# Optimization experiments

Measured on AMD Instinct MI355X. Metric: run time of the kernel, lower is better.

The kernel has to match this reference:

```python
import jax, jax.numpy as jnp
import numpy as np

DIM = 2048
N_HEADS = 32
N_KV_HEADS = 8
HEAD_DIM = 64
BATCH = 2
SEQ = 2048
N_REP = N_HEADS // N_KV_HEADS
SCALE = HEAD_DIM ** -0.5
ROPE_BASE = 10000.0


def setup_inputs() -> dict:
    key = jax.random.key(0)
    ks = jax.random.split(key, 5)
    x = jax.random.normal(ks[0], (BATCH, SEQ, DIM), dtype=jnp.float32)
    # weights stored as (in, out) so projection is x @ W
    Wq = jax.random.normal(ks[1], (DIM, N_HEADS * HEAD_DIM), dtype=jnp.float32) * (DIM ** -0.5)
    Wk = jax.random.normal(ks[2], (DIM, N_KV_HEADS * HEAD_DIM), dtype=jnp.float32) * (DIM ** -0.5)
    Wv = jax.random.normal(ks[3], (DIM, N_KV_HEADS * HEAD_DIM), dtype=jnp.float32) * (DIM ** -0.5)
    Wo = jax.random.normal(ks[4], (N_HEADS * HEAD_DIM, DIM), dtype=jnp.float32) * ((N_HEADS * HEAD_DIM) ** -0.5)
    # RoPE tables (seq, head_dim)
    inv_freq = 1.0 / (ROPE_BASE ** (jnp.arange(0, HEAD_DIM, 2, dtype=jnp.float32) / HEAD_DIM))
    t = jnp.arange(SEQ, dtype=jnp.float32)
    freqs = jnp.outer(t, inv_freq)                      # (S, D/2)
    emb = jnp.concatenate([freqs, freqs], axis=-1)      # (S, D)
    cos = jnp.cos(emb)
    sin = jnp.sin(emb)
    # additive causal mask (1,1,S,S)
    neg = jnp.finfo(jnp.float32).min
    causal = jnp.tril(jnp.ones((SEQ, SEQ), dtype=bool))
    attention_mask = jnp.where(causal, 0.0, neg)[None, None, :, :].astype(jnp.float32)
    return {"x": x, "Wq": Wq, "Wk": Wk, "Wv": Wv, "Wo": Wo,
            "cos": cos, "sin": sin, "attention_mask": attention_mask}


def _rotate_half(u):
    h = u.shape[-1] // 2
    return jnp.concatenate([-u[..., h:], u[..., :h]], axis=-1)


def reference(x, Wq, Wk, Wv, Wo, cos, sin, attention_mask):
    b, s, _ = x.shape
    q = (x @ Wq).reshape(b, s, N_HEADS, HEAD_DIM)
    k = (x @ Wk).reshape(b, s, N_KV_HEADS, HEAD_DIM)
    v = (x @ Wv).reshape(b, s, N_KV_HEADS, HEAD_DIM)
    # RoPE, broadcast over head dim (unsqueeze_dim=2)
    c = cos[None, :, None, :]
    sn = sin[None, :, None, :]
    q = q * c + _rotate_half(q) * sn
    k = k * c + _rotate_half(k) * sn
    # repeat KV heads for GQA: (b,s,kvh,d) -> (b,s,h,d)
    k = jnp.repeat(k, N_REP, axis=2)
    v = jnp.repeat(v, N_REP, axis=2)
    # (b,h,s,d)
    q = q.transpose(0, 2, 1, 3)
    k = k.transpose(0, 2, 1, 3)
    v = v.transpose(0, 2, 1, 3)
    scores = jnp.einsum("bhqd,bhkd->bhqk", q, k) * SCALE + attention_mask
    attn = jax.nn.softmax(scores.astype(jnp.float32), axis=-1).astype(q.dtype)
    out = jnp.einsum("bhqk,bhkd->bhqd", attn, v)
    out = out.transpose(0, 2, 1, 3).reshape(b, s, N_HEADS * HEAD_DIM)
    return out @ Wo
```

## Files before the change

### kernel.cpp

```cpp
#include <hip/hip_runtime.h>
#include <hip/hip_bf16.h>

typedef unsigned short u16;
typedef unsigned int   u32;
typedef __bf16 bf16_t;
typedef bf16_t bf16x8 __attribute__((ext_vector_type(8)));
typedef u16    u16x8  __attribute__((ext_vector_type(8)));
typedef float  f32x4  __attribute__((ext_vector_type(4)));

#define DIM  2048
#define SEQ  2048
#define BATCH 2
#define NH   32
#define NKVH 8
#define HD   64
#define KVDIM (NKVH*HD)
#define NQKV (DIM + 2*KVDIM)
#define SCALE 0.125f

__device__ __forceinline__ float b2f(u16 u) {
  union { u32 i; float f; } v; v.i = ((u32)u) << 16; return v.f;
}
__device__ __forceinline__ u16 f2b(float f) {
  union { float f; u32 i; } v; v.f = f;
  u32 x = v.i;
  return (u16)((x + 0x7fffu + ((x >> 16) & 1u)) >> 16);
}
__device__ __forceinline__ u32 pkbf2(float a, float b) {
  __hip_bfloat162 h = __float22bfloat162_rn(float2{a, b});
  union { __hip_bfloat162 h; u32 u; } v; v.h = h; return v.u;
}
__device__ __forceinline__ int probe_bf16(const u32* probe) { return probe[0] != 0u; }
__device__ __forceinline__ float ext_ld(const void* p, long idx, int mode_bf16) {
  return mode_bf16 ? b2f(((const u16*)p)[idx]) : ((const float*)p)[idx];
}
__device__ __forceinline__ void gload_lds16(const u16* g, u16* l) {
  __builtin_amdgcn_global_load_lds((const __attribute__((address_space(1))) void*)g,
                                   (__attribute__((address_space(3))) void*)l, 16, 0, 0);
}

__global__ void cast_x(const void* __restrict__ in, u16* __restrict__ out,
                       const u32* __restrict__ probe) {
  int mode = probe_bf16(probe);
  long base = ((long)blockIdx.x * 256 + threadIdx.x) * 8;
  if (mode) {
    *(uint4*)&out[base] = *(const uint4*)((const u16*)in + base);
  } else {
    float4 f0 = *(const float4*)((const float*)in + base);
    float4 f1 = *(const float4*)((const float*)in + base + 4);
    u16x8 t;
    t[0] = f2b(f0.x); t[1] = f2b(f0.y); t[2] = f2b(f0.z); t[3] = f2b(f0.w);
    t[4] = f2b(f1.x); t[5] = f2b(f1.y); t[6] = f2b(f1.z); t[7] = f2b(f1.w);
    *(u16x8*)&out[base] = t;
  }
}

__global__ void transpose_qkv(const void* __restrict__ Wq, const void* __restrict__ Wk,
                              const void* __restrict__ Wv, u16* __restrict__ out,
                              const u32* __restrict__ probe) {
  int mode = probe_bf16(probe);
  __shared__ u16 t[32][33];
  int xt = blockIdx.x;
  const void* in; int C, c0, obase;
  if (xt < 64)      { in = Wq; C = DIM;   c0 = xt * 32;        obase = 0; }
  else if (xt < 80) { in = Wk; C = KVDIM; c0 = (xt - 64) * 32; obase = DIM; }
  else              { in = Wv; C = KVDIM; c0 = (xt - 80) * 32; obase = DIM + KVDIM; }
  int r0 = blockIdx.y * 32;
  int tx = threadIdx.x, ty = threadIdx.y;
#pragma unroll
  for (int i = 0; i < 32; i += 8)
    t[ty + i][tx] = mode ? ((const u16*)in)[(long)(r0 + ty + i) * C + c0 + tx]
                         : f2b(((const float*)in)[(long)(r0 + ty + i) * C + c0 + tx]);
  __syncthreads();
#pragma unroll
  for (int i = 0; i < 32; i += 8)
    out[(long)(obase + c0 + ty + i) * DIM + r0 + tx] = t[tx][ty + i];
}

__global__ void transpose_w(const void* __restrict__ in, u16* __restrict__ out,
                            int R, int C, const u32* __restrict__ probe) {
  int mode = probe_bf16(probe);
  __shared__ u16 t[32][33];
  int c0 = blockIdx.x * 32, r0 = blockIdx.y * 32;
  int tx = threadIdx.x, ty = threadIdx.y;
#pragma unroll
  for (int i = 0; i < 32; i += 8)
    t[ty + i][tx] = mode ? ((const u16*)in)[(long)(r0 + ty + i) * C + c0 + tx]
                         : f2b(((const float*)in)[(long)(r0 + ty + i) * C + c0 + tx]);
  __syncthreads();
#pragma unroll
  for (int i = 0; i < 32; i += 8)
    out[(long)(c0 + ty + i) * R + r0 + tx] = t[tx][ty + i];
}

__global__ void rope_both(u16* __restrict__ Qb, u16* __restrict__ Kb,
                          const void* __restrict__ cosb, const void* __restrict__ sinb,
                          const u32* __restrict__ probe) {
  int mode = probe_bf16(probe);
  long gid = (long)blockIdx.x * 256 + threadIdx.x;
  const long NQp = (long)BATCH * SEQ * NH * 32;
  u16* base_p; int n_heads; long t; float osc;
  if (gid < NQp) { base_p = Qb; n_heads = NH; t = gid; osc = SCALE; }
  else           { base_p = Kb; n_heads = NKVH; t = gid - NQp; osc = 1.0f; }
  int pair = t & 31;
  long t2 = t >> 5;
  int h = (int)(t2 % n_heads);
  long row = t2 / n_heads;
  int s = (int)(row & (SEQ - 1));
  long base = row * (n_heads * HD) + h * HD + pair;
  float q0 = b2f(base_p[base]), q1 = b2f(base_p[base + 32]);
  float c0 = ext_ld(cosb, (long)s * HD + pair, mode);
  float c1 = ext_ld(cosb, (long)s * HD + pair + 32, mode);
  float s0 = ext_ld(sinb, (long)s * HD + pair, mode);
  float s1 = ext_ld(sinb, (long)s * HD + pair + 32, mode);
  base_p[base]      = f2b((q0 * c0 - q1 * s0) * osc);
  base_p[base + 32] = f2b((q1 * c1 + q0 * s1) * osc);
}


__launch_bounds__(256)
__global__ void gemm_qkv(const void* __restrict__ A, const u16* __restrict__ Bt,
                         u16* __restrict__ Qb, u16* __restrict__ Kb, u16* __restrict__ Vt,
                         int a_half, const u32* __restrict__ probe) {
  int mode = a_half || probe_bf16(probe);
  __shared__ __align__(16) u16 As[128 * 32];
  __shared__ __align__(16) u16 Bs[128 * 32];
  int tid = threadIdx.x, lane = tid & 63, wv = tid >> 6;
  int l16 = lane & 15, q = lane >> 4;
  int bm0 = blockIdx.y * 128, bn0 = blockIdx.x * 128;
  int mbase = (wv & 1) * 64, nbase = (wv >> 1) * 64;
  int c0 = tid, c1 = tid + 256;
  int r0 = c0 >> 2, s0 = (c0 & 3) ^ ((r0 >> 1) & 3);
  int r1 = c1 >> 2, s1 = (c1 & 3) ^ ((r1 >> 1) & 3);
  const int K = DIM;
  long aoff0 = (long)(bm0 + r0) * K + s0 * 8;
  long aoff1 = (long)(bm0 + r1) * K + s1 * 8;
  long boff0 = (long)(bn0 + r0) * K + s0 * 8;
  long boff1 = (long)(bn0 + r1) * K + s1 * 8;
  int rsw = (q ^ ((l16 >> 1) & 3)) * 8;
  f32x4 acc[4][4] = {};
  for (int k0 = 0; k0 < K; k0 += 32) {
    __syncthreads();
    if (mode) {
      gload_lds16((const u16*)A + aoff0 + k0, &As[wv * 512]);
      gload_lds16((const u16*)A + aoff1 + k0, &As[2048 + wv * 512]);
    } else {
      const float* Af = (const float*)A;
      float4 f0 = *(const float4*)(Af + aoff0 + k0);
      float4 f1 = *(const float4*)(Af + aoff0 + k0 + 4);
      u16x8 t;
      t[0] = f2b(f0.x); t[1] = f2b(f0.y); t[2] = f2b(f0.z); t[3] = f2b(f0.w);
      t[4] = f2b(f1.x); t[5] = f2b(f1.y); t[6] = f2b(f1.z); t[7] = f2b(f1.w);
      *(u16x8*)&As[c0 * 8] = t;
      float4 g0 = *(const float4*)(Af + aoff1 + k0);
      float4 g1 = *(const float4*)(Af + aoff1 + k0 + 4);
      u16x8 u;
      u[0] = f2b(g0.x); u[1] = f2b(g0.y); u[2] = f2b(g0.z); u[3] = f2b(g0.w);
      u[4] = f2b(g1.x); u[5] = f2b(g1.y); u[6] = f2b(g1.z); u[7] = f2b(g1.w);
      *(u16x8*)&As[c1 * 8] = u;
    }
    gload_lds16(Bt + boff0 + k0, &Bs[wv * 512]);
    gload_lds16(Bt + boff1 + k0, &Bs[2048 + wv * 512]);
    __syncthreads();
    bf16x8 af[4], bfr[4];
#pragma unroll
    for (int mi = 0; mi < 4; mi++)
      af[mi] = *(const bf16x8*)&As[(mbase + mi * 16 + l16) * 32 + rsw];
#pragma unroll
    for (int ni = 0; ni < 4; ni++)
      bfr[ni] = *(const bf16x8*)&Bs[(nbase + ni * 16 + l16) * 32 + rsw];
#pragma unroll
    for (int mi = 0; mi < 4; mi++)
#pragma unroll
      for (int ni = 0; ni < 4; ni++)
        acc[mi][ni] = __builtin_amdgcn_mfma_f32_16x16x32_bf16(
            af[mi], bfr[ni], acc[mi][ni], 0, 0, 0);
  }
  if (bn0 < DIM + KVDIM) {
    u16* Cb; int ldc, ncol0;
    if (bn0 < DIM) { Cb = Qb; ldc = DIM; ncol0 = bn0; }
    else           { Cb = Kb; ldc = KVDIM; ncol0 = bn0 - DIM; }
#pragma unroll
    for (int mi = 0; mi < 4; mi++)
#pragma unroll
      for (int ni = 0; ni < 4; ni++)
#pragma unroll
        for (int r = 0; r < 4; r++) {
          int m = bm0 + mbase + mi * 16 + q * 4 + r;
          int n = ncol0 + nbase + ni * 16 + l16;
          Cb[(long)m * ldc + n] = f2b(acc[mi][ni][r]);
        }
  } else {
    int vcol0 = bn0 - DIM - KVDIM;
#pragma unroll
    for (int mi = 0; mi < 4; mi++)
#pragma unroll
      for (int ni = 0; ni < 4; ni++) {
        int vcol = vcol0 + nbase + ni * 16 + l16;
        int kvh2 = vcol >> 6, d = vcol & 63;
        int m = bm0 + mbase + mi * 16 + q * 4;
        int bb = m >> 11, s = m & (SEQ - 1);
        uint2 w;
        w.x = pkbf2(acc[mi][ni][0], acc[mi][ni][1]);
        w.y = pkbf2(acc[mi][ni][2], acc[mi][ni][3]);
        *(uint2*)&Vt[((long)(bb * NKVH + kvh2) * HD + d) * SEQ + s] = w;
      }
  }
}

__launch_bounds__(256)
__global__ void gemm_ao(const u16* __restrict__ A, const u16* __restrict__ Bt,
                        void* __restrict__ C, const u32* __restrict__ probe) {
  int mode = probe_bf16(probe);
  __shared__ __align__(16) u16 As[128 * 32];
  __shared__ __align__(16) u16 Bs[128 * 32];
  int tid = threadIdx.x, lane = tid & 63, wv = tid >> 6;
  int l16 = lane & 15, q = lane >> 4;
  int bm0 = blockIdx.y * 128, bn0 = blockIdx.x * 128;
  int mbase = (wv & 1) * 64, nbase = (wv >> 1) * 64;
  int c0 = tid, c1 = tid + 256;
  int r0 = c0 >> 2, s0 = (c0 & 3) ^ ((r0 >> 1) & 3);
  int r1 = c1 >> 2, s1 = (c1 & 3) ^ ((r1 >> 1) & 3);
  const int K = DIM;
  long aoff0 = (long)(bm0 + r0) * K + s0 * 8;
  long aoff1 = (long)(bm0 + r1) * K + s1 * 8;
  long boff0 = (long)(bn0 + r0) * K + s0 * 8;
  long boff1 = (long)(bn0 + r1) * K + s1 * 8;
  int rsw = (q ^ ((l16 >> 1) & 3)) * 8;
  f32x4 acc[4][4] = {};
  for (int k0 = 0; k0 < K; k0 += 32) {
    __syncthreads();
    gload_lds16(A + aoff0 + k0, &As[wv * 512]);
    gload_lds16(A + aoff1 + k0, &As[2048 + wv * 512]);
    gload_lds16(Bt + boff0 + k0, &Bs[wv * 512]);
    gload_lds16(Bt + boff1 + k0, &Bs[2048 + wv * 512]);
    __syncthreads();
    bf16x8 af[4], bfr[4];
#pragma unroll
    for (int mi = 0; mi < 4; mi++)
      af[mi] = *(const bf16x8*)&As[(mbase + mi * 16 + l16) * 32 + rsw];
#pragma unroll
    for (int ni = 0; ni < 4; ni++)
      bfr[ni] = *(const bf16x8*)&Bs[(nbase + ni * 16 + l16) * 32 + rsw];
#pragma unroll
    for (int mi = 0; mi < 4; mi++)
#pragma unroll
      for (int ni = 0; ni < 4; ni++)
        acc[mi][ni] = __builtin_amdgcn_mfma_f32_16x16x32_bf16(
            af[mi], bfr[ni], acc[mi][ni], 0, 0, 0);
  }
#pragma unroll
  for (int mi = 0; mi < 4; mi++)
#pragma unroll
    for (int ni = 0; ni < 4; ni++)
#pragma unroll
      for (int r = 0; r < 4; r++) {
        int m = bm0 + mbase + mi * 16 + q * 4 + r;
        int n = bn0 + nbase + ni * 16 + l16;
        if (mode) ((u16*)C)[(long)m * DIM + n] = f2b(acc[mi][ni][r]);
        else      ((float*)C)[(long)m * DIM + n] = acc[mi][ni][r];
      }
}

__launch_bounds__(256, 4)
__global__ void attn_kernel(const u16* __restrict__ Q, const u16* __restrict__ K,
                            const u16* __restrict__ Vt, u16* __restrict__ AO) {
  __shared__ __align__(16) u16 Ks[64 * 64];
  __shared__ __align__(16) u16 Vs[64 * 64];
  __shared__ __align__(16) u16 Ps[4][16 * 64];
  int tid = threadIdx.x, lane = tid & 63, wv = tid >> 6;
  int l16 = lane & 15, q = lane >> 4;
  int i = blockIdx.x;
  int bh = blockIdx.y;
  int b = bh >> 5, h = bh & 31, kvh = h >> 2;
  const u16* Kp = K + (long)b * SEQ * KVDIM + kvh * HD;
  const u16* Vp = Vt + (long)(b * NKVH + kvh) * HD * SEQ;

  int cA = tid, cB = tid + 256;
  int rA = cA >> 3, bA = (cA & 7) ^ (rA & 7);
  int rB = cB >> 3, bB = (cB & 7) ^ (rB & 7);
  const u16* kSrcA = Kp + (long)rA * KVDIM + bA * 8;
  const u16* kSrcB = Kp + (long)rB * KVDIM + bB * 8;
  const u16* vSrcA = Vp + (long)rA * SEQ + bA * 8;
  const u16* vSrcB = Vp + (long)rB * SEQ + bB * 8;
  u16* kDstA = &Ks[(wv * 64 + lane) * 8];
  u16* kDstB = &Ks[(256 + wv * 64 + lane) * 8];
  u16* vDstA = &Vs[(wv * 64 + lane) * 8];
  u16* vDstB = &Vs[(256 + wv * 64 + lane) * 8];

  int e = l16 & 7;
  int off0 = (q ^ e) * 8;
  int off1 = ((4 + q) ^ e) * 8;

  bf16x8 ones;
#pragma unroll
  for (int j = 0; j < 8; j++) ones[j] = (bf16_t)1.0f;

#pragma unroll
  for (int ph = 0; ph < 2; ph++) {
    int t = ph ? (31 - i) : i;
    int qbase = t * 64 + wv * 16;
    const u16* Qp = Q + (long)(b * SEQ + qbase) * DIM + h * HD;
    bf16x8 aq0 = *(const bf16x8*)&Qp[l16 * DIM + q * 8];
    bf16x8 aq1 = *(const bf16x8*)&Qp[l16 * DIM + 32 + q * 8];
    f32x4 o_acc[4] = {};
    f32x4 l_acc = {};
    int qrow = qbase + l16;

    for (int kt = 0; kt <= t; kt++) {
      long kk = (long)kt * 64;
      __syncthreads();
      gload_lds16(kSrcA + kk * KVDIM, kDstA);
      gload_lds16(kSrcB + kk * KVDIM, kDstB);
      gload_lds16(vSrcA + kk, vDstA);
      gload_lds16(vSrcB + kk, vDstB);
      __syncthreads();

      f32x4 sc[4];
#pragma unroll
      for (int ni = 0; ni < 4; ni++) {
        bf16x8 bk0 = *(const bf16x8*)&Ks[(ni * 16 + l16) * 64 + off0];
        bf16x8 bk1 = *(const bf16x8*)&Ks[(ni * 16 + l16) * 64 + off1];
        f32x4 z = {};
        z = __builtin_amdgcn_mfma_f32_16x16x32_bf16(bk0, aq0, z, 0, 0, 0);
        z = __builtin_amdgcn_mfma_f32_16x16x32_bf16(bk1, aq1, z, 0, 0, 0);
        sc[ni] = z;
      }
      if (kt == t) {
#pragma unroll
        for (int ni = 0; ni < 4; ni++)
#pragma unroll
          for (int r = 0; r < 4; r++) {
            int kv = (int)kk + ni * 16 + q * 4 + r;
            float p = __expf(sc[ni][r]);
            sc[ni][r] = (kv <= qrow) ? p : 0.f;
          }
      } else {
#pragma unroll
        for (int ni = 0; ni < 4; ni++)
#pragma unroll
          for (int r = 0; r < 4; r++) sc[ni][r] = __expf(sc[ni][r]);
      }
#pragma unroll
      for (int ni = 0; ni < 4; ni++) {
        uint2 w;
        w.x = pkbf2(sc[ni][0], sc[ni][1]);
        w.y = pkbf2(sc[ni][2], sc[ni][3]);
        int pblk = (2 * ni + (q >> 1)) ^ e;
        *(uint2*)&Ps[wv][l16 * 64 + pblk * 8 + (q & 1) * 4] = w;
      }
      bf16x8 ap0 = *(const bf16x8*)&Ps[wv][l16 * 64 + off0];
      bf16x8 ap1 = *(const bf16x8*)&Ps[wv][l16 * 64 + off1];
      l_acc = __builtin_amdgcn_mfma_f32_16x16x32_bf16(ap0, ones, l_acc, 0, 0, 0);
      l_acc = __builtin_amdgcn_mfma_f32_16x16x32_bf16(ap1, ones, l_acc, 0, 0, 0);
#pragma unroll
      for (int di = 0; di < 4; di++) {
        bf16x8 bv0 = *(const bf16x8*)&Vs[(di * 16 + l16) * 64 + off0];
        bf16x8 bv1 = *(const bf16x8*)&Vs[(di * 16 + l16) * 64 + off1];
        o_acc[di] = __builtin_amdgcn_mfma_f32_16x16x32_bf16(ap0, bv0, o_acc[di], 0, 0, 0);
        o_acc[di] = __builtin_amdgcn_mfma_f32_16x16x32_bf16(ap1, bv1, o_acc[di], 0, 0, 0);
      }
    }
    long obase = (long)(b * SEQ + qbase + q * 4) * DIM + h * HD;
#pragma unroll
    for (int r = 0; r < 4; r++) {
      float inv = 1.0f / l_acc[r];
#pragma unroll
      for (int di = 0; di < 4; di++)
        AO[obase + (long)r * DIM + di * 16 + l16] = f2b(o_acc[di][r] * inv);
    }
  }
}

extern "C" void kernel_launch(void* const* d_in, const int* in_sizes, int n_in,
                              void* d_out, int out_size, void* d_ws, size_t ws_size,
                              hipStream_t stream) {
  const void* x    = d_in[0];
  const void* Wq   = d_in[1];
  const void* Wk   = d_in[2];
  const void* Wv   = d_in[3];
  const void* Wo   = d_in[4];
  const void* cosb = d_in[5];
  const void* sinb = d_in[6];
  const u32*  probe = (const u32*)d_in[7];

  u16* WqkvT = (u16*)d_ws;
  u16* WoT = WqkvT + (size_t)NQKV * DIM;
  u16* Qb  = WoT + (size_t)DIM * DIM;
  u16* Kb  = Qb  + (size_t)BATCH * SEQ * DIM;
  u16* Vt  = Kb  + (size_t)BATCH * SEQ * KVDIM;
  u16* xb  = Vt  + (size_t)BATCH * NKVH * HD * SEQ;
  u16* AO  = Qb;

  size_t need_xb = ((size_t)(xb - WqkvT) + (size_t)BATCH * SEQ * DIM) * sizeof(u16);
  int use_xb = ws_size >= need_xb;

  dim3 blk32(32, 8);
  transpose_qkv<<<dim3(96, 64), blk32, 0, stream>>>(Wq, Wk, Wv, WqkvT, probe);
  transpose_w<<<dim3(DIM / 32, DIM / 32), blk32, 0, stream>>>(Wo, WoT, DIM, DIM, probe);

  int M = BATCH * SEQ;
  if (use_xb) {
    cast_x<<<(M * DIM) / (256 * 8), 256, 0, stream>>>(x, xb, probe);
    gemm_qkv<<<dim3(NQKV / 128, M / 128), 256, 0, stream>>>(xb, WqkvT, Qb, Kb, Vt, 1, probe);
  } else {
    gemm_qkv<<<dim3(NQKV / 128, M / 128), 256, 0, stream>>>(x, WqkvT, Qb, Kb, Vt, 0, probe);
  }

  long rope_slots = (long)M * NH * 32 + (long)M * NKVH * 32;
  rope_both<<<(int)(rope_slots / 256), 256, 0, stream>>>(Qb, Kb, cosb, sinb, probe);

  attn_kernel<<<dim3(16, BATCH * NH), 256, 0, stream>>>(Qb, Kb, Vt, AO);

  gemm_ao<<<dim3(DIM / 128, M / 128), 256, 0, stream>>>(AO, WoT, d_out, probe);
}
```

Measured before the change: 327.2 us.

## Replace QKV and output GEMMs with 8-wave double-buffered pipelined GEMM core

Adds a templated 512-thread GEMM core with 256-wide N tiles, BK=64, LDS double buffering, interleaved async global-to-LDS stages, explicit vmcnt waits, sched barriers and setprio around MFMA quads. The QKV projection and the output projection both use it, replacing the simple single-buffered 128x128 kernels that synchronised twice per 32-wide K step. cast_x now skips work when inputs are already bf16, and the QKV GEMM reads x directly in that case. The change aims to hide load latency and raise MFMA utilisation, at the cost of more LDS per block and tighter hand-tuned wait counts that must match the issue order.

New measurement: 343.8 us. 1.05x slower.

```diff
diff --git a/kernel.cpp b/kernel.cpp
--- a/kernel.cpp
+++ b/kernel.cpp
@@ -42,17 +42,14 @@
 __global__ void cast_x(const void* __restrict__ in, u16* __restrict__ out,
                        const u32* __restrict__ probe) {
   int mode = probe_bf16(probe);
+  if (mode) return;
   long base = ((long)blockIdx.x * 256 + threadIdx.x) * 8;
-  if (mode) {
-    *(uint4*)&out[base] = *(const uint4*)((const u16*)in + base);
-  } else {
-    float4 f0 = *(const float4*)((const float*)in + base);
-    float4 f1 = *(const float4*)((const float*)in + base + 4);
-    u16x8 t;
-    t[0] = f2b(f0.x); t[1] = f2b(f0.y); t[2] = f2b(f0.z); t[3] = f2b(f0.w);
-    t[4] = f2b(f1.x); t[5] = f2b(f1.y); t[6] = f2b(f1.z); t[7] = f2b(f1.w);
-    *(u16x8*)&out[base] = t;
-  }
+  float4 f0 = *(const float4*)((const float*)in + base);
+  float4 f1 = *(const float4*)((const float*)in + base + 4);
+  u16x8 t;
+  t[0] = f2b(f0.x); t[1] = f2b(f0.y); t[2] = f2b(f0.z); t[3] = f2b(f0.w);
+  t[4] = f2b(f1.x); t[5] = f2b(f1.y); t[6] = f2b(f1.z); t[7] = f2b(f1.w);
+  *(u16x8*)&out[base] = t;
 }
 
 __global__ void transpose_qkv(const void* __restrict__ Wq, const void* __restrict__ Wk,
@@ -117,6 +114,221 @@
   base_p[base + 32] = f2b((q1 * c1 + q0 * s1) * osc);
 }
 
+
+#define WAITV(N) asm volatile("s_waitcnt vmcnt(%0)" :: "n"(N) : "memory")
+#define WAITL()  asm volatile("s_waitcnt lgkmcnt(0)" ::: "memory")
+#define BARR()   __builtin_amdgcn_s_barrier()
+#define SCHEDB() __builtin_amdgcn_sched_barrier(0)
+#define PRIO1()  __builtin_amdgcn_s_setprio(1)
+#define PRIO0()  __builtin_amdgcn_s_setprio(0)
+
+#define STAGE_A(h, bufi, kt) do { _Pragma("unroll") \
+  for (int _j = 0; _j < AL; ++_j) \
+    gload_lds16(Ax + aSrcOff[h][_j] + (kt) * 64, (u16*)&As[(bufi) * (BM * 64) + aDst[h][_j]]); } while (0)
+
+#define STAGE_B(h, bufi, kt) do { _Pragma("unroll") \
+  for (int _j = 0; _j < 2; ++_j) \
+    gload_lds16(Bt + bSrcOff[h][_j] + (kt) * 64, (u16*)&Bs[(bufi) * (256 * 64) + bDst[h][_j]]); } while (0)
+
+#define LDA_HALF(Lp, mh) do { _Pragma("unroll") \
+  for (int _m = 0; _m < MH2; ++_m) { \
+    const u16* _r = (Lp) + (wm * WM + (mh) * (WM / 2) + _m * 16 + l16) * 64; \
+    af[_m][0] = *(const bf16x8*)&_r[sw0]; \
+    af[_m][1] = *(const bf16x8*)&_r[sw1]; } } while (0)
+
+#define LDB_HALF(Lp, nh) do { _Pragma("unroll") \
+  for (int _n = 0; _n < 2; ++_n) { \
+    const u16* _r = (Lp) + (wn * 64 + (nh) * 32 + _n * 16 + l16) * 64; \
+    bfr[nh][_n][0] = *(const bf16x8*)&_r[sw0]; \
+    bfr[nh][_n][1] = *(const bf16x8*)&_r[sw1]; } } while (0)
+
+#define MFMA_Q(mh, nh) do { _Pragma("unroll") \
+  for (int _m = 0; _m < MH2; ++_m) \
+    _Pragma("unroll") \
+    for (int _n = 0; _n < 2; ++_n) { \
+      f32x4 _z = acc[(mh) * MH2 + _m][(nh) * 2 + _n]; \
+      _z = __builtin_amdgcn_mfma_f32_16x16x32_bf16(af[_m][0], bfr[nh][_n][0], _z, 0, 0, 0); \
+      _z = __builtin_amdgcn_mfma_f32_16x16x32_bf16(af[_m][1], bfr[nh][_n][1], _z, 0, 0, 0); \
+      acc[(mh) * MH2 + _m][(nh) * 2 + _n] = _z; } } while (0)
+
+template<int BM, int EPI>
+__device__ __forceinline__ void gemm8_core(const u16* __restrict__ Ax, const u16* __restrict__ Bt,
+                                           u16* __restrict__ Qb, u16* __restrict__ Kb,
+                                           u16* __restrict__ Vt, void* __restrict__ Cout,
+                                           const u32* __restrict__ probe) {
+  constexpr int WM  = BM / 2;
+  constexpr int MI  = WM / 16;
+  constexpr int MH2 = MI / 2;
+  constexpr int AL  = BM / 128;
+  constexpr int VM_A = 6 + 3 * AL;
+  constexpr int VM_B = 4 + 4 * AL;
+  constexpr int K = DIM;
+  __shared__ __align__(16) u16 As[2 * BM * 64];
+  __shared__ __align__(16) u16 Bs[2 * 256 * 64];
+
+  int tid = threadIdx.x, lane = tid & 63, wv = tid >> 6;
+  int l16 = lane & 15, q = lane >> 4;
+  int wm = wv >> 2, wn = wv & 3;
+  int bm0 = blockIdx.y * BM, bn0 = blockIdx.x * 256;
+
+  int srow = lane >> 3;
+  int scolb = ((lane & 7) ^ srow) * 8;
+  int e7 = l16 & 7;
+  int sw0 = (q ^ e7) * 8, sw1 = ((4 + q) ^ e7) * 8;
+
+  int aSrcOff[2][AL], aDst[2][AL];
+#pragma unroll
+  for (int h = 0; h < 2; ++h)
+#pragma unroll
+    for (int j = 0; j < AL; ++j) {
+      int g = wv * AL + j;
+      int rb = (BM == 256) ? ((g >> 3) * 128 + h * 64 + (g & 7) * 8)
+                           : ((g >> 2) * 64 + h * 32 + (g & 3) * 8);
+      aSrcOff[h][j] = (bm0 + rb + srow) * K + scolb;
+      aDst[h][j] = rb * 64 + lane * 8;
+    }
+  int bSrcOff[2][2], bDst[2][2];
+#pragma unroll
+  for (int h = 0; h < 2; ++h)
+#pragma unroll
+    for (int j = 0; j < 2; ++j) {
+      int g = wv * 2 + j;
+      int rb = (g >> 2) * 64 + h * 32 + (g & 3) * 8;
+      bSrcOff[h][j] = (bn0 + rb + srow) * K + scolb;
+      bDst[h][j] = rb * 64 + lane * 8;
+    }
+
+  const u16* As0 = As;  const u16* As1 = As + BM * 64;
+  const u16* Bs0 = Bs;  const u16* Bs1 = Bs + 256 * 64;
+
+  f32x4 acc[MI][4] = {};
+  bf16x8 af[MH2][2];
+  bf16x8 bfr[2][2][2];
+
+  STAGE_A(0, 0, 0);
+  STAGE_B(0, 0, 0);
+  STAGE_B(1, 0, 0);
+  STAGE_A(1, 0, 0);
+  STAGE_A(0, 1, 1);
+  STAGE_B(0, 1, 1);
+  STAGE_B(1, 1, 1);
+
+#pragma unroll 1
+  for (int i = 0; i < 16; ++i) {
+    int te = 2 * i + 2; if (te > 31) te = 31;
+    int to = 2 * i + 3; if (to > 31) to = 31;
+    SCHEDB();
+    STAGE_A(1, 1, 2 * i + 1);
+    WAITV(VM_A); BARR(); SCHEDB();
+    LDA_HALF(As0, 0); LDB_HALF(Bs0, 0);
+    WAITL(); BARR();
+    PRIO1(); MFMA_Q(0, 0); PRIO0();
+    SCHEDB();
+    STAGE_A(0, 0, te);
+    WAITV(VM_B); BARR(); SCHEDB();
+    LDB_HALF(Bs0, 1);
+    WAITL(); BARR();
+    PRIO1(); MFMA_Q(0, 1); PRIO0();
+    SCHEDB();
+    STAGE_B(0, 0, te);
+    WAITV(VM_A); BARR(); SCHEDB();
+    LDA_HALF(As0, 1);
+    WAITL(); BARR();
+    PRIO1(); MFMA_Q(1, 0); PRIO0();
+    SCHEDB();
+    STAGE_B(1, 0, te);
+    PRIO1(); MFMA_Q(1, 1); PRIO0();
+    SCHEDB();
+    STAGE_A(1, 0, te);
+    WAITV(VM_A); BARR(); SCHEDB();
+    LDA_HALF(As1, 0); LDB_HALF(Bs1, 0);
+    WAITL(); BARR();
+    PRIO1(); MFMA_Q(0, 0); PRIO0();
+    SCHEDB();
+    STAGE_A(0, 1, to);
+    WAITV(VM_B); BARR(); SCHEDB();
+    LDB_HALF(Bs1, 1);
+    WAITL(); BARR();
+    PRIO1(); MFMA_Q(0, 1); PRIO0();
+    SCHEDB();
+    STAGE_B(0, 1, to);
+    WAITV(VM_A); BARR(); SCHEDB();
+    LDA_HALF(As1, 1);
+    WAITL(); BARR();
+    PRIO1(); MFMA_Q(1, 0); PRIO0();
+    SCHEDB();
+    STAGE_B(1, 1, to);
+    PRIO1(); MFMA_Q(1, 1); PRIO0();
+  }
+
+  if constexpr (EPI == 0) {
+    if (bn0 < DIM) {
+#pragma unroll
+      for (int mi = 0; mi < MI; ++mi)
+#pragma unroll
+        for (int ni = 0; ni < 4; ++ni)
+#pragma unroll
+          for (int r = 0; r < 4; ++r) {
+            int m = bm0 + wm * WM + mi * 16 + q * 4 + r;
+            int n = bn0 + wn * 64 + ni * 16 + l16;
+            Qb[(long)m * DIM + n] = f2b(acc[mi][ni][r]);
+          }
+    } else if (bn0 < DIM + KVDIM) {
+#pragma unroll
+      for (int mi = 0; mi < MI; ++mi)
+#pragma unroll
+        for (int ni = 0; ni < 4; ++ni)
+#pragma unroll
+          for (int r = 0; r < 4; ++r) {
+            int m = bm0 + wm * WM + mi * 16 + q * 4 + r;
+            int n = bn0 - DIM + wn * 64 + ni * 16 + l16;
+            Kb[(long)m * KVDIM + n] = f2b(acc[mi][ni][r]);
+          }
+    } else {
+#pragma unroll
+      for (int mi = 0; mi < MI; ++mi)
+#pragma unroll
+        for (int ni = 0; ni < 4; ++ni) {
+          int vcol = bn0 - (DIM + KVDIM) + wn * 64 + ni * 16 + l16;
+          int kvh2 = vcol >> 6, d = vcol & 63;
+          int m0 = bm0 + wm * WM + mi * 16 + q * 4;
+          int bb = m0 >> 11, s = m0 & (SEQ - 1);
+          uint2 w;
+          w.x = pkbf2(acc[mi][ni][0], acc[mi][ni][1]);
+          w.y = pkbf2(acc[mi][ni][2], acc[mi][ni][3]);
+          *(uint2*)&Vt[((long)(bb * NKVH + kvh2) * HD + d) * SEQ + s] = w;
+        }
+    }
+  } else {
+    int mode = probe_bf16(probe);
+#pragma unroll
+    for (int mi = 0; mi < MI; ++mi)
+#pragma unroll
+      for (int ni = 0; ni < 4; ++ni)
+#pragma unroll
+        for (int r = 0; r < 4; ++r) {
+          int m = bm0 + wm * WM + mi * 16 + q * 4 + r;
+          int n = bn0 + wn * 64 + ni * 16 + l16;
+          long idx = (long)m * DIM + n;
+          if (mode) ((u16*)Cout)[idx] = f2b(acc[mi][ni][r]);
+          else      ((float*)Cout)[idx] = acc[mi][ni][r];
+        }
+  }
+}
+
+__global__ __launch_bounds__(512, 2)
+void gemm_qkv8(const void* __restrict__ x, const u16* __restrict__ xb,
+               const u16* __restrict__ Bt, u16* __restrict__ Qb, u16* __restrict__ Kb,
+               u16* __restrict__ Vt, const u32* __restrict__ probe) {
+  const u16* Ax = probe_bf16(probe) ? (const u16*)x : xb;
+  gemm8_core<256, 0>(Ax, Bt, Qb, Kb, Vt, nullptr, probe);
+}
+
+__global__ __launch_bounds__(512, 2)
+void gemm_ao8(const u16* __restrict__ A, const u16* __restrict__ Bt,
+              void* __restrict__ C, const u32* __restrict__ probe) {
+  gemm8_core<128, 1>(A, Bt, nullptr, nullptr, nullptr, C, probe);
+}
 
 __launch_bounds__(256)
 __global__ void gemm_qkv(const void* __restrict__ A, const u16* __restrict__ Bt,
@@ -208,60 +420,6 @@
   }
 }
 
-__launch_bounds__(256)
-__global__ void gemm_ao(const u16* __restrict__ A, const u16* __restrict__ Bt,
-                        void* __restrict__ C, const u32* __restrict__ probe) {
-  int mode = probe_bf16(probe);
-  __shared__ __align__(16) u16 As[128 * 32];
-  __shared__ __align__(16) u16 Bs[128 * 32];
-  int tid = threadIdx.x, lane = tid & 63, wv = tid >> 6;
-  int l16 = lane & 15, q = lane >> 4;
-  int bm0 = blockIdx.y * 128, bn0 = blockIdx.x * 128;
-  int mbase = (wv & 1) * 64, nbase = (wv >> 1) * 64;
-  int c0 = tid, c1 = tid + 256;
-  int r0 = c0 >> 2, s0 = (c0 & 3) ^ ((r0 >> 1) & 3);
-  int r1 = c1 >> 2, s1 = (c1 & 3) ^ ((r1 >> 1) & 3);
-  const int K = DIM;
-  long aoff0 = (long)(bm0 + r0) * K + s0 * 8;
-  long aoff1 = (long)(bm0 + r1) * K + s1 * 8;
-  long boff0 = (long)(bn0 + r0) * K + s0 * 8;
-  long boff1 = (long)(bn0 + r1) * K + s1 * 8;
-  int rsw = (q ^ ((l16 >> 1) & 3)) * 8;
-  f32x4 acc[4][4] = {};
-  for (int k0 = 0; k0 < K; k0 += 32) {
-    __syncthreads();
-    gload_lds16(A + aoff0 + k0, &As[wv * 512]);
-    gload_lds16(A + aoff1 + k0, &As[2048 + wv * 512]);
-    gload_lds16(Bt + boff0 + k0, &Bs[wv * 512]);
-    gload_lds16(Bt + boff1 + k0, &Bs[2048 + wv * 512]);
-    __syncthreads();
-    bf16x8 af[4], bfr[4];
-#pragma unroll
-    for (int mi = 0; mi < 4; mi++)
-      af[mi] = *(const bf16x8*)&As[(mbase + mi * 16 + l16) * 32 + rsw];
-#pragma unroll
-    for (int ni = 0; ni < 4; ni++)
-      bfr[ni] = *(const bf16x8*)&Bs[(nbase + ni * 16 + l16) * 32 + rsw];
-#pragma unroll
-    for (int mi = 0; mi < 4; mi++)
-#pragma unroll
-      for (int ni = 0; ni < 4; ni++)
-        acc[mi][ni] = __builtin_amdgcn_mfma_f32_16x16x32_bf16(
-            af[mi], bfr[ni], acc[mi][ni], 0, 0, 0);
-  }
-#pragma unroll
-  for (int mi = 0; mi < 4; mi++)
-#pragma unroll
-    for (int ni = 0; ni < 4; ni++)
-#pragma unroll
-      for (int r = 0; r < 4; r++) {
-        int m = bm0 + mbase + mi * 16 + q * 4 + r;
-        int n = bn0 + nbase + ni * 16 + l16;
-        if (mode) ((u16*)C)[(long)m * DIM + n] = f2b(acc[mi][ni][r]);
-        else      ((float*)C)[(long)m * DIM + n] = acc[mi][ni][r];
-      }
-}
-
 __launch_bounds__(256, 4)
 __global__ void attn_kernel(const u16* __restrict__ Q, const u16* __restrict__ K,
                             const u16* __restrict__ Vt, u16* __restrict__ AO) {
@@ -402,7 +560,7 @@
   int M = BATCH * SEQ;
   if (use_xb) {
     cast_x<<<(M * DIM) / (256 * 8), 256, 0, stream>>>(x, xb, probe);
-    gemm_qkv<<<dim3(NQKV / 128, M / 128), 256, 0, stream>>>(xb, WqkvT, Qb, Kb, Vt, 1, probe);
+    gemm_qkv8<<<dim3(NQKV / 256, M / 256), 512, 0, stream>>>(x, xb, WqkvT, Qb, Kb, Vt, probe);
   } else {
     gemm_qkv<<<dim3(NQKV / 128, M / 128), 256, 0, stream>>>(x, WqkvT, Qb, Kb, Vt, 0, probe);
   }
@@ -412,5 +570,5 @@
 
   attn_kernel<<<dim3(16, BATCH * NH), 256, 0, stream>>>(Qb, Kb, Vt, AO);
 
-  gemm_ao<<<dim3(DIM / 128, M / 128), 256, 0, stream>>>(AO, WoT, d_out, probe);
-}
+  gemm_ao8<<<dim3(DIM / 256, M / 128), 512, 0, stream>>>(AO, WoT, d_out, probe);
+}
```

## Fuse RoPE into QKV GEMM epilogue and double-buffer K/V tiles in attention

Applied to the files above, without the earlier changes.

Removes the standalone RoPE kernel by applying rotation and the Q scale inside the QKV GEMM epilogue. This works because each wave's 64-column tile covers one full head, so the d and d+32 pairs sit in acc[ni] and acc[ni+2]. The attention kernel now double-buffers the K/V LDS tiles, prefetching the next tile while the current one is computed, which also drops one barrier per iteration. In exchange, LDS use in the attention kernel grows, which may lower occupancy under the launch bound of 4 blocks, and the epilogue does extra cos/sin loads.

Result: slower. 353.6 us (+8.1%).

```diff
diff --git a/kernel.cpp b/kernel.cpp
--- a/kernel.cpp
+++ b/kernel.cpp
@@ -93,36 +93,14 @@
     out[(long)(c0 + ty + i) * R + r0 + tx] = t[tx][ty + i];
 }
 
-__global__ void rope_both(u16* __restrict__ Qb, u16* __restrict__ Kb,
-                          const void* __restrict__ cosb, const void* __restrict__ sinb,
-                          const u32* __restrict__ probe) {
-  int mode = probe_bf16(probe);
-  long gid = (long)blockIdx.x * 256 + threadIdx.x;
-  const long NQp = (long)BATCH * SEQ * NH * 32;
-  u16* base_p; int n_heads; long t; float osc;
-  if (gid < NQp) { base_p = Qb; n_heads = NH; t = gid; osc = SCALE; }
-  else           { base_p = Kb; n_heads = NKVH; t = gid - NQp; osc = 1.0f; }
-  int pair = t & 31;
-  long t2 = t >> 5;
-  int h = (int)(t2 % n_heads);
-  long row = t2 / n_heads;
-  int s = (int)(row & (SEQ - 1));
-  long base = row * (n_heads * HD) + h * HD + pair;
-  float q0 = b2f(base_p[base]), q1 = b2f(base_p[base + 32]);
-  float c0 = ext_ld(cosb, (long)s * HD + pair, mode);
-  float c1 = ext_ld(cosb, (long)s * HD + pair + 32, mode);
-  float s0 = ext_ld(sinb, (long)s * HD + pair, mode);
-  float s1 = ext_ld(sinb, (long)s * HD + pair + 32, mode);
-  base_p[base]      = f2b((q0 * c0 - q1 * s0) * osc);
-  base_p[base + 32] = f2b((q1 * c1 + q0 * s1) * osc);
-}
-
 
 __launch_bounds__(256)
 __global__ void gemm_qkv(const void* __restrict__ A, const u16* __restrict__ Bt,
                          u16* __restrict__ Qb, u16* __restrict__ Kb, u16* __restrict__ Vt,
-                         int a_half, const u32* __restrict__ probe) {
-  int mode = a_half || probe_bf16(probe);
+                         int a_half, const void* __restrict__ cosb,
+                         const void* __restrict__ sinb, const u32* __restrict__ probe) {
+  int pmode = probe_bf16(probe);
+  int mode = a_half || pmode;
   __shared__ __align__(16) u16 As[128 * 32];
   __shared__ __align__(16) u16 Bs[128 * 32];
   int tid = threadIdx.x, lane = tid & 63, wv = tid >> 6;
@@ -177,19 +155,26 @@
             af[mi], bfr[ni], acc[mi][ni], 0, 0, 0);
   }
   if (bn0 < DIM + KVDIM) {
-    u16* Cb; int ldc, ncol0;
-    if (bn0 < DIM) { Cb = Qb; ldc = DIM; ncol0 = bn0; }
-    else           { Cb = Kb; ldc = KVDIM; ncol0 = bn0 - DIM; }
-#pragma unroll
-    for (int mi = 0; mi < 4; mi++)
-#pragma unroll
-      for (int ni = 0; ni < 4; ni++)
-#pragma unroll
-        for (int r = 0; r < 4; r++) {
-          int m = bm0 + mbase + mi * 16 + q * 4 + r;
-          int n = ncol0 + nbase + ni * 16 + l16;
-          Cb[(long)m * ldc + n] = f2b(acc[mi][ni][r]);
+    u16* Cb; int ldc, ncol0; float osc;
+    if (bn0 < DIM) { Cb = Qb; ldc = DIM; ncol0 = bn0; osc = SCALE; }
+    else           { Cb = Kb; ldc = KVDIM; ncol0 = bn0 - DIM; osc = 1.0f; }
+#pragma unroll
+    for (int mi = 0; mi < 4; mi++)
+#pragma unroll
+      for (int r = 0; r < 4; r++) {
+        int m = bm0 + mbase + mi * 16 + q * 4 + r;
+        int st = m & (SEQ - 1);
+#pragma unroll
+        for (int ni = 0; ni < 2; ni++) {
+          int d = ni * 16 + l16;
+          float c  = ext_ld(cosb, (long)st * HD + d, pmode);
+          float sn = ext_ld(sinb, (long)st * HD + d, pmode);
+          float a = acc[mi][ni][r], b = acc[mi][ni + 2][r];
+          long base = (long)m * ldc + ncol0 + nbase + d;
+          Cb[base]      = f2b((a * c - b * sn) * osc);
+          Cb[base + 32] = f2b((b * c + a * sn) * osc);
         }
+      }
   } else {
     int vcol0 = bn0 - DIM - KVDIM;
 #pragma unroll
@@ -265,8 +250,8 @@
 __launch_bounds__(256, 4)
 __global__ void attn_kernel(const u16* __restrict__ Q, const u16* __restrict__ K,
                             const u16* __restrict__ Vt, u16* __restrict__ AO) {
-  __shared__ __align__(16) u16 Ks[64 * 64];
-  __shared__ __align__(16) u16 Vs[64 * 64];
+  __shared__ __align__(16) u16 Ks[2 * 64 * 64];
+  __shared__ __align__(16) u16 Vs[2 * 64 * 64];
   __shared__ __align__(16) u16 Ps[4][16 * 64];
   int tid = threadIdx.x, lane = tid & 63, wv = tid >> 6;
   int l16 = lane & 15, q = lane >> 4;
@@ -307,20 +292,32 @@
     f32x4 l_acc = {};
     int qrow = qbase + l16;
 
+    __syncthreads();
+    gload_lds16(kSrcA, kDstA);
+    gload_lds16(kSrcB, kDstB);
+    gload_lds16(vSrcA, vDstA);
+    gload_lds16(vSrcB, vDstB);
+    int curo = 0;
+
     for (int kt = 0; kt <= t; kt++) {
+      __syncthreads();
+      if (kt < t) {
+        long kk2 = (long)(kt + 1) * 64;
+        int nxt = curo ^ 4096;
+        gload_lds16(kSrcA + kk2 * KVDIM, kDstA + nxt);
+        gload_lds16(kSrcB + kk2 * KVDIM, kDstB + nxt);
+        gload_lds16(vSrcA + kk2, vDstA + nxt);
+        gload_lds16(vSrcB + kk2, vDstB + nxt);
+      }
+      const u16* Ksb = &Ks[curo];
+      const u16* Vsb = &Vs[curo];
       long kk = (long)kt * 64;
-      __syncthreads();
-      gload_lds16(kSrcA + kk * KVDIM, kDstA);
-      gload_lds16(kSrcB + kk * KVDIM, kDstB);
-      gload_lds16(vSrcA + kk, vDstA);
-      gload_lds16(vSrcB + kk, vDstB);
-      __syncthreads();
 
       f32x4 sc[4];
 #pragma unroll
       for (int ni = 0; ni < 4; ni++) {
-        bf16x8 bk0 = *(const bf16x8*)&Ks[(ni * 16 + l16) * 64 + off0];
-        bf16x8 bk1 = *(const bf16x8*)&Ks[(ni * 16 + l16) * 64 + off1];
+        bf16x8 bk0 = *(const bf16x8*)&Ksb[(ni * 16 + l16) * 64 + off0];
+        bf16x8 bk1 = *(const bf16x8*)&Ksb[(ni * 16 + l16) * 64 + off1];
         f32x4 z = {};
         z = __builtin_amdgcn_mfma_f32_16x16x32_bf16(bk0, aq0, z, 0, 0, 0);
         z = __builtin_amdgcn_mfma_f32_16x16x32_bf16(bk1, aq1, z, 0, 0, 0);
@@ -355,11 +352,12 @@
       l_acc = __builtin_amdgcn_mfma_f32_16x16x32_bf16(ap1, ones, l_acc, 0, 0, 0);
 #pragma unroll
       for (int di = 0; di < 4; di++) {
-        bf16x8 bv0 = *(const bf16x8*)&Vs[(di * 16 + l16) * 64 + off0];
-        bf16x8 bv1 = *(const bf16x8*)&Vs[(di * 16 + l16) * 64 + off1];
+        bf16x8 bv0 = *(const bf16x8*)&Vsb[(di * 16 + l16) * 64 + off0];
+        bf16x8 bv1 = *(const bf16x8*)&Vsb[(di * 16 + l16) * 64 + off1];
         o_acc[di] = __builtin_amdgcn_mfma_f32_16x16x32_bf16(ap0, bv0, o_acc[di], 0, 0, 0);
         o_acc[di] = __builtin_amdgcn_mfma_f32_16x16x32_bf16(ap1, bv1, o_acc[di], 0, 0, 0);
       }
+      curo ^= 4096;
     }
     long obase = (long)(b * SEQ + qbase + q * 4) * DIM + h * HD;
 #pragma unroll
@@ -402,13 +400,12 @@
   int M = BATCH * SEQ;
   if (use_xb) {
     cast_x<<<(M * DIM) / (256 * 8), 256, 0, stream>>>(x, xb, probe);
-    gemm_qkv<<<dim3(NQKV / 128, M / 128), 256, 0, stream>>>(xb, WqkvT, Qb, Kb, Vt, 1, probe);
+    gemm_qkv<<<dim3(NQKV / 128, M / 128), 256, 0, stream>>>(xb, WqkvT, Qb, Kb, Vt, 1,
+                                                            cosb, sinb, probe);
   } else {
-    gemm_qkv<<<dim3(NQKV / 128, M / 128), 256, 0, stream>>>(x, WqkvT, Qb, Kb, Vt, 0, probe);
-  }
-
-  long rope_slots = (long)M * NH * 32 + (long)M * NKVH * 32;
-  rope_both<<<(int)(rope_slots / 256), 256, 0, stream>>>(Qb, Kb, cosb, sinb, probe);
+    gemm_qkv<<<dim3(NQKV / 128, M / 128), 256, 0, stream>>>(x, WqkvT, Qb, Kb, Vt, 0,
+                                                            cosb, sinb, probe);
+  }
 
   attn_kernel<<<dim3(16, BATCH * NH), 256, 0, stream>>>(Qb, Kb, Vt, AO);
 
```
